# Kernel optimization log

Measured on AMD Instinct MI355X. Metric: run time of the kernel, lower is better.

Reference implementation:

```python
import jax, jax.numpy as jnp
import numpy as np

B, S, E, H = 4, 1024, 1024, 16
HD = E // H  # head_dim = 64
MAX_SEQ = 1024  # rel positions span [-(MAX_SEQ-1), MAX_SEQ-1]


def setup_inputs() -> dict:
    key = jax.random.key(0)
    ks = jax.random.split(key, 12)
    std_e = 1.0 / np.sqrt(E)
    std_h = 1.0 / np.sqrt(HD)
    inp = {
        "x": jax.random.normal(ks[0], (B, S, E), dtype=jnp.float32),
        # torch nn.Linear weights are [out, in]; y = x @ W.T + b
        "Wq": jax.random.uniform(ks[1], (E, E), jnp.float32, -std_e, std_e),
        "bq": jax.random.uniform(ks[2], (E,), jnp.float32, -std_e, std_e),
        "Wk": jax.random.uniform(ks[3], (E, E), jnp.float32, -std_e, std_e),
        "bk": jax.random.uniform(ks[4], (E,), jnp.float32, -std_e, std_e),
        "Wv": jax.random.uniform(ks[5], (E, E), jnp.float32, -std_e, std_e),
        "bv": jax.random.uniform(ks[6], (E,), jnp.float32, -std_e, std_e),
        "Wo": jax.random.uniform(ks[7], (E, E), jnp.float32, -std_e, std_e),
        "bo": jax.random.uniform(ks[8], (E,), jnp.float32, -std_e, std_e),
        # pos_key_proj: Linear(head_dim, head_dim, bias=False)
        "Wp": jax.random.uniform(ks[9], (HD, HD), jnp.float32, -std_h, std_h),
        # learned relative position table [2*max_seq_len-1, head_dim]
        "rel_table": jax.random.normal(ks[10], (2 * MAX_SEQ - 1, HD), dtype=jnp.float32),
    }
    return inp


def _rel_shift(pos_scores):
    # pos_scores: [B, H, S, 2S-1] -> [B, H, S, S]
    # result[..., i, j] = pos_scores[..., i, (S-1) - i + j]
    s = pos_scores.shape[-2]
    idx = (s - 1) - jnp.arange(s)[:, None] + jnp.arange(s)[None, :]  # [S, S]
    return jnp.take_along_axis(pos_scores, idx[None, None, :, :], axis=-1)


def reference(x, Wq, bq, Wk, bk, Wv, bv, Wo, bo, Wp, rel_table):
    scale = 1.0 / np.sqrt(HD)
    Q = (x @ Wq.T + bq).reshape(B, S, H, HD).transpose(0, 2, 1, 3)  # [B,H,S,HD]
    K = (x @ Wk.T + bk).reshape(B, S, H, HD).transpose(0, 2, 1, 3)
    V = (x @ Wv.T + bv).reshape(B, S, H, HD).transpose(0, 2, 1, 3)

    # rel_pos_encoding(S): slice centered at MAX_SEQ-1 covering 2S-1 positions
    center = MAX_SEQ - 1
    rel_emb = rel_table[center - (S - 1): center + S]  # [2S-1, HD]
    rel_key = rel_emb @ Wp.T                            # [2S-1, HD]

    content = jnp.einsum("bhqd,bhkd->bhqk", Q, K) * scale       # [B,H,S,S]
    pos = jnp.einsum("bhqd,pd->bhqp", Q, rel_key) * scale       # [B,H,S,2S-1]
    scores = content + _rel_shift(pos)                          # [B,H,S,S]

    probs = jax.nn.softmax(scores, axis=-1)
    ctx = jnp.einsum("bhqk,bhkd->bhqd", probs, V)               # [B,H,S,HD]
    ctx = ctx.transpose(0, 2, 1, 3).reshape(B, S, E)
    return ctx @ Wo.T + bo
```

## Files before the change

### kernel.cpp

```cpp
#include <hip/hip_runtime.h>
#include <hip/hip_bf16.h>

#define B_   4
#define S_   1024
#define E_   1024
#define H_   16
#define HD_  64

typedef float  f32x4  __attribute__((ext_vector_type(4)));
typedef short  bf16x8 __attribute__((ext_vector_type(8)));
typedef short  bf16x4 __attribute__((ext_vector_type(4)));

__device__ __forceinline__ float bf2f(short u) {
  union { unsigned int i; float f; } v;
  v.i = ((unsigned int)(unsigned short)u) << 16;
  return v.f;
}
__device__ __forceinline__ short f2bf(float f) {
  unsigned int x = __float_as_uint(f);
  x = x + 0x7fffu + ((x >> 16) & 1u);
  return (short)(x >> 16);
}
__device__ __forceinline__ bf16x8 ld_cvt8(const float* __restrict__ p) {
  const f32x4 a = *(const f32x4*)p;
  const f32x4 b = *(const f32x4*)(p + 4);
  bf16x8 r;
  r[0] = f2bf(a[0]); r[1] = f2bf(a[1]); r[2] = f2bf(a[2]); r[3] = f2bf(a[3]);
  r[4] = f2bf(b[0]); r[5] = f2bf(b[1]); r[6] = f2bf(b[2]); r[7] = f2bf(b[3]);
  return r;
}

__device__ __forceinline__ void gload_lds16(const short* g, short* l) {
  __builtin_amdgcn_global_load_lds(
      (const __attribute__((address_space(1))) void*)g,
      (__attribute__((address_space(3))) void*)l, 16, 0, 0);
}

__global__ __launch_bounds__(256) void cvt_f32_bf16(
    const float* __restrict__ src, short* __restrict__ dst, int n)
{
  const int i = (blockIdx.x * 256 + threadIdx.x) * 4;
  if (i < n) {
    const f32x4 v = *(const f32x4*)(src + i);
    bf16x4 o;
    o[0] = f2bf(v[0]); o[1] = f2bf(v[1]); o[2] = f2bf(v[2]); o[3] = f2bf(v[3]);
    *(bf16x4*)(dst + i) = o;
  }
}

__global__ __launch_bounds__(256) void cvt7_f32_bf16(
    const float* __restrict__ w0, const float* __restrict__ w1,
    const float* __restrict__ w2, const float* __restrict__ x,
    short* __restrict__ WB, short* __restrict__ xbf)
{
  const int NW = E_ * E_;
  const int y = blockIdx.y;
  const float* src;
  short* dst;
  if (y < 3) { src = (y == 0) ? w0 : (y == 1) ? w1 : w2; dst = WB + (size_t)y * NW; }
  else       { src = x + (size_t)(y - 3) * NW;           dst = xbf + (size_t)(y - 3) * NW; }
  const int i = (blockIdx.x * 256 + threadIdx.x) * 4;
  const f32x4 v = *(const f32x4*)(src + i);
  bf16x4 o;
  o[0] = f2bf(v[0]); o[1] = f2bf(v[1]); o[2] = f2bf(v[2]); o[3] = f2bf(v[3]);
  *(bf16x4*)(dst + i) = o;
}

template<int TM, int OUTF32>
__global__ __launch_bounds__(256) void gemm_bt(
    const short* __restrict__ A,
    const short* __restrict__ W0, const short* __restrict__ W1, const short* __restrict__ W2,
    const float* __restrict__ b0, const float* __restrict__ b1, const float* __restrict__ b2,
    void* __restrict__ C0v, void* __restrict__ C1v, void* __restrict__ C2v, int vz)
{
  constexpr int NJ = (TM == 128) ? 4 : 2;
  __shared__ short As[TM * 32];
  __shared__ short Bs[128 * 32];

  const int tid  = threadIdx.x;
  const int lane = tid & 63;
  const int wave = tid >> 6;
  const int quad = lane >> 4;
  const int l15  = lane & 15;
  const int wmb  = (TM == 128) ? (wave >> 1) * 64 : 0;
  const int wnb  = (TM == 128) ? (wave & 1) * 64 : wave * 32;
  const int m0   = blockIdx.y * TM;
  const int n0   = blockIdx.x * 128;
  const int z    = blockIdx.z;

  const short* W  = (z == 0) ? W0 : (z == 1) ? W1 : W2;
  const float* bb = (z == 0) ? b0 : (z == 1) ? b1 : b2;
  void*        Cv = (z == 0) ? C0v : (z == 1) ? C1v : C2v;

  const int trow = tid >> 2;
  const int tc   = tid & 3;

  f32x4 acc[4][NJ] = {};

  for (int k0 = 0; k0 < E_; k0 += 32) {
#pragma unroll
    for (int n = 0; n < TM / 64; ++n) {
      const int row  = trow + n * 64;
      const int srcc = tc ^ ((row >> 1) & 3);
      gload_lds16(A + (size_t)(m0 + row) * E_ + k0 + srcc * 8, &As[n * 2048 + tid * 8]);
    }
#pragma unroll
    for (int n = 0; n < 2; ++n) {
      const int row  = trow + n * 64;
      const int srcc = tc ^ ((row >> 1) & 3);
      gload_lds16(W + (size_t)(n0 + row) * E_ + k0 + srcc * 8, &Bs[n * 2048 + tid * 8]);
    }
    __syncthreads();

    bf16x8 af[4], bfr[NJ];
#pragma unroll
    for (int i = 0; i < 4; ++i) {
      const int row = wmb + i * 16 + l15;
      const int pc  = quad ^ ((row >> 1) & 3);
      af[i] = *(bf16x8*)&As[row * 32 + pc * 8];
    }
#pragma unroll
    for (int j = 0; j < NJ; ++j) {
      const int row = wnb + j * 16 + l15;
      const int pc  = quad ^ ((row >> 1) & 3);
      bfr[j] = *(bf16x8*)&Bs[row * 32 + pc * 8];
    }
#pragma unroll
    for (int i = 0; i < 4; ++i)
#pragma unroll
      for (int j = 0; j < NJ; ++j)
        acc[i][j] = __builtin_amdgcn_mfma_f32_16x16x32_bf16(af[i], bfr[j], acc[i][j], 0, 0, 0);
    __syncthreads();
  }

  if (TM == 128 && z == vz) {
    const int mtb = m0 + wmb;
    const int bq  = mtb >> 10;
    const int kt  = (mtb >> 6) & 15;
    short* Cs = (short*)Cv;
#pragma unroll
    for (int j = 0; j < NJ; ++j) {
      const int n = n0 + wnb + j * 16 + l15;
      const float bv = bb[n];
      const int h = (n >> 6) & 15;
      const int d = n & 63;
      bf16x8 lo, hi;
#pragma unroll
      for (int e = 0; e < 8; ++e) {
        lo[e] = f2bf(acc[e & 3][j][e >> 2] + bv);
        hi[e] = f2bf(acc[e & 3][j][(e >> 2) + 2] + bv);
      }
      const size_t off = ((size_t)((bq * 16 + h) * 64 + d)) * 1024 + kt * 64 + quad * 16;
      *(bf16x8*)(Cs + off)     = lo;
      *(bf16x8*)(Cs + off + 8) = hi;
    }
  } else {
#pragma unroll
    for (int j = 0; j < NJ; ++j) {
      const int n = n0 + wnb + j * 16 + l15;
      const float bv = bb[n];
#pragma unroll
      for (int i = 0; i < 4; ++i) {
        const int m = m0 + wmb + i * 16 + quad * 4;
#pragma unroll
        for (int r = 0; r < 4; ++r) {
          const float v = acc[i][j][r] + bv;
          if (OUTF32) ((float*)Cv)[(size_t)(m + r) * E_ + n] = v;
          else        ((short*)Cv)[(size_t)(m + r) * E_ + n] = f2bf(v);
        }
      }
    }
  }
}

__global__ __launch_bounds__(256) void relkey_mfma(
    const float* __restrict__ rel, const float* __restrict__ Wp, short* __restrict__ RKw)
{
  const int tid  = threadIdx.x;
  const int lane = tid & 63;
  const int wv   = tid >> 6;
  const int quad = lane >> 4;
  const int l15  = lane & 15;
  const int p0   = blockIdx.x * 64 + wv * 16;

  bf16x8 af[2];
  {
    int prow = p0 + l15; if (prow > 2046) prow = 2046;
    const float* ap = rel + (size_t)prow * 64 + quad * 8;
    af[0] = ld_cvt8(ap);
    af[1] = ld_cvt8(ap + 32);
  }
  f32x4 acc[4] = {};
#pragma unroll
  for (int nt = 0; nt < 4; ++nt) {
    const float* bp = Wp + (size_t)(nt * 16 + l15) * 64 + quad * 8;
    acc[nt] = __builtin_amdgcn_mfma_f32_16x16x32_bf16(af[0], ld_cvt8(bp),      acc[nt], 0, 0, 0);
    acc[nt] = __builtin_amdgcn_mfma_f32_16x16x32_bf16(af[1], ld_cvt8(bp + 32), acc[nt], 0, 0, 0);
  }
#pragma unroll
  for (int r = 0; r < 4; ++r) {
    const int p = p0 + quad * 4 + r;
    if (p < 2047)
#pragma unroll
      for (int nt = 0; nt < 4; ++nt)
        RKw[(size_t)p * 64 + nt * 16 + l15] = f2bf(acc[nt][r]);
  }
}

__global__ __launch_bounds__(512, 4) void attn_kernel(
    const short* __restrict__ Qw, const short* __restrict__ Kw,
    const short* __restrict__ Vtg, const short* __restrict__ RKw,
    short* __restrict__ Cw)
{
  __shared__ short Ks[64][72];
  __shared__ short Vt[64][72];
  __shared__ short RKs[256][72];
  __shared__ short Ps[8][16][72];

  const int tid  = threadIdx.x;
  const int lane = tid & 63;
  const int wv   = tid >> 6;
  const int quad = lane >> 4;
  const int l15  = lane & 15;

  const int lid  = blockIdx.x;
  const int pair = (lid & 7) * 8 + (lid >> 6);
  const int qt   = (lid >> 3) & 7;
  const int b    = pair >> 4;
  const int h    = pair & 15;
  const int bh   = pair;
  const int q0   = qt * 128;
  const int qw0  = q0 + wv * 16;
  const int jb   = 112 - 16 * wv;
  const int pbase0 = S_ - 128 - q0;

  bf16x8 qf[2];
  {
    const size_t base = (size_t)(b * S_ + qw0 + l15) * E_ + h * HD_ + quad * 8;
    qf[0] = *(const bf16x8*)(Qw + base);
    qf[1] = *(const bf16x8*)(Qw + base + 32);
  }

  f32x4 oacc[4] = {};
  float lsum[4] = {0.f, 0.f, 0.f, 0.f};

  const float fs = 0.125f * 1.44269504088896340736f;

  const int sr  = tid >> 3;
  const int sc8 = (tid & 7) * 8;

  {
    *(bf16x8*)&Ks[sr][sc8] =
        *(const bf16x8*)(Kw + (size_t)(b * S_ + sr) * E_ + h * HD_ + sc8);
    *(bf16x8*)&Vt[sr][sc8] =
        *(const bf16x8*)(Vtg + (size_t)(bh * 64 + sr) * 1024 + sc8);
#pragma unroll
    for (int jj = 0; jj < 3; ++jj) {
      const int c = tid + jj * 512;
      const int row = c >> 3, ch = (c & 7) * 8;
      int p = pbase0 + row; p = (p > 2046) ? 2046 : p;
      *(bf16x8*)&RKs[row][ch] = *(const bf16x8*)(RKw + (size_t)p * 64 + ch);
    }
    __syncthreads();
  }

#pragma unroll 1
  for (int kt = 0; kt < 16; ++kt) {
    bf16x8 kreg, vreg, rkreg;
    const bool havekv = (kt < 15);
    const bool haverk = (kt < 15);
    if (havekv) {
      kreg = *(const bf16x8*)(Kw + (size_t)(b * S_ + (kt + 1) * 64 + sr) * E_ + h * HD_ + sc8);
      vreg = *(const bf16x8*)(Vtg + (size_t)(bh * 64 + sr) * 1024 + (kt + 1) * 64 + sc8);
    }
    if (haverk) {
      int p = pbase0 + 64 * (kt + 3) + sr; if (p > 2046) p = 2046;
      rkreg = *(const bf16x8*)(RKw + (size_t)p * 64 + sc8);
    }

    f32x4 sc[4] = {};
#pragma unroll
    for (int s = 0; s < 2; ++s) {
#pragma unroll
      for (int kk = 0; kk < 4; ++kk) {
        bf16x8 bf = *(bf16x8*)&Ks[kk*16 + l15][s*32 + quad*8];
        sc[kk] = __builtin_amdgcn_mfma_f32_16x16x32_bf16(qf[s], bf, sc[kk], 0, 0, 0);
      }
    }

    f32x4 ta[5] = {};
#pragma unroll
    for (int jt = 0; jt < 5; ++jt) {
      const int off  = jb + jt * 16;
      const int slot = (kt + (off >> 6)) & 3;
      const int prow = slot * 64 + (off & 63);
#pragma unroll
      for (int s = 0; s < 2; ++s) {
        bf16x8 bf = *(bf16x8*)&RKs[prow + l15][s*32 + quad*8];
        ta[jt] = __builtin_amdgcn_mfma_f32_16x16x32_bf16(qf[s], bf, ta[jt], 0, 0, 0);
      }
    }

    float p[4][4];
#pragma unroll
    for (int r = 0; r < 4; ++r) {
      const int i16 = quad*4 + r;
      const int d   = 15 + l15 - i16;
      const int srcLane = (quad << 4) | (d & 15);
      float sj[5];
#pragma unroll
      for (int jt = 0; jt < 5; ++jt) sj[jt] = __shfl(ta[jt][r], srcLane, 64);
      const bool hi = (d >= 16);
#pragma unroll
      for (int kk = 0; kk < 4; ++kk) {
        const float t = hi ? sj[kk+1] : sj[kk];
        const float sv = fminf((sc[kk][r] + t) * fs, 108.f);
        const float pv = exp2f(sv - 12.f);
        p[kk][r] = pv;
        lsum[r] += pv;
      }
    }

#pragma unroll
    for (int r = 0; r < 4; ++r) {
      bf16x4 pw;
      pw[0] = f2bf(p[0][r]); pw[1] = f2bf(p[1][r]);
      pw[2] = f2bf(p[2][r]); pw[3] = f2bf(p[3][r]);
      *(bf16x4*)&Ps[wv][quad*4 + r][l15*4] = pw;
    }

#pragma unroll
    for (int ks = 0; ks < 2; ++ks) {
      bf16x8 pa = *(bf16x8*)&Ps[wv][l15][ks*32 + quad*8];
#pragma unroll
      for (int dt = 0; dt < 4; ++dt) {
        bf16x8 vb = *(bf16x8*)&Vt[dt*16 + l15][ks*32 + quad*8];
        oacc[dt] = __builtin_amdgcn_mfma_f32_16x16x32_bf16(pa, vb, oacc[dt], 0, 0, 0);
      }
    }

    __syncthreads();
    if (havekv) {
      *(bf16x8*)&Ks[sr][sc8] = kreg;
      *(bf16x8*)&Vt[sr][sc8] = vreg;
    }
    if (haverk) {
      *(bf16x8*)&RKs[((kt + 3) & 3) * 64 + sr][sc8] = rkreg;
    }
    __syncthreads();
  }

#pragma unroll
  for (int off = 1; off <= 8; off <<= 1)
#pragma unroll
    for (int r = 0; r < 4; ++r)
      lsum[r] += __shfl_xor(lsum[r], off, 64);

#pragma unroll
  for (int r = 0; r < 4; ++r) {
    const float inv = 1.0f / lsum[r];
    const size_t row = (size_t)(b * S_ + qw0 + quad*4 + r) * E_ + h * HD_;
#pragma unroll
    for (int dt = 0; dt < 4; ++dt)
      Cw[row + dt*16 + l15] = f2bf(oacc[dt][r] * inv);
  }
}

__global__ void fill_kernel(float* __restrict__ out, int n, float val) {
  for (int i = blockIdx.x * blockDim.x + threadIdx.x; i < n; i += gridDim.x * blockDim.x)
    out[i] = val;
}

extern "C" void kernel_launch(void* const* d_in, const int* in_sizes, int n_in,
                              void* d_out, int out_size, void* d_ws, size_t ws_size,
                              hipStream_t stream)
{
  const size_t WS_NEEDED = 33816448;
  if (ws_size < WS_NEEDED) {
    fill_kernel<<<1024, 256, 0, stream>>>((float*)d_out, out_size, 0.25f);
    return;
  }
  if (n_in != 11 || in_sizes[10] != 2047 * 64) {
    fill_kernel<<<1024, 256, 0, stream>>>((float*)d_out, out_size, 0.75f);
    return;
  }

  const float* x   = (const float*)d_in[0];
  const float* Wq  = (const float*)d_in[1];
  const float* bq  = (const float*)d_in[2];
  const float* Wk  = (const float*)d_in[3];
  const float* bk  = (const float*)d_in[4];
  const float* Wv  = (const float*)d_in[5];
  const float* bv  = (const float*)d_in[6];
  const float* Wo  = (const float*)d_in[7];
  const float* bo  = (const float*)d_in[8];
  const float* Wp  = (const float*)d_in[9];
  const float* rel = (const float*)d_in[10];

  char* ws = (char*)d_ws;
  short* Qws = (short*)(ws);
  short* Kws = (short*)(ws + 8388608);
  short* Vtg = (short*)(ws + 16777216);
  short* WB  = (short*)(ws + 25165824);
  short* ctx = (short*)(ws + 25165824);
  short* WoB = (short*)(ws + 8388608);
  short* RKw = (short*)(ws + 33554432);
  short* xbf = (short*)d_out;

  const int NW = E_ * E_;

  cvt7_f32_bf16<<<dim3(1024, 7), dim3(256), 0, stream>>>(Wq, Wk, Wv, x, WB, xbf);

  gemm_bt<128, 0><<<dim3(8, 32, 3), dim3(256), 0, stream>>>(
      xbf, WB, WB + NW, WB + 2 * NW, bq, bk, bv, Qws, Kws, Vtg, 2);

  relkey_mfma<<<dim3(32), dim3(256), 0, stream>>>(rel, Wp, RKw);

  attn_kernel<<<dim3(512), dim3(512), 0, stream>>>(Qws, Kws, Vtg, RKw, ctx);

  cvt_f32_bf16<<<dim3(NW / 1024), dim3(256), 0, stream>>>(Wo, WoB, NW);

  gemm_bt<64, 1><<<dim3(8, 64, 1), dim3(256), 0, stream>>>(
      ctx, WoB, WoB, WoB, bo, bo, bo, d_out, d_out, d_out, -1);
}
```

Baseline: 256.6 us.

## Fuse QKV projections into one GEMM sharing A tiles, swizzle block order

Replaces the three separate Q/K/V GEMM launches, indexed by blockIdx.z, with one kernel. Each block loads one 128-row tile of x and multiplies it against 64-column slices of all three weight matrices, so each A tile is reused three times instead of being reloaded per projection. Block indices are also remapped so neighbouring blocks share A rows for better L2 locality, and the output projection GEMM gets the same swizzled 1D grid. The cost is more accumulator registers per thread (3x4x2 tiles, launch bounds asking for 3 blocks per SM) and narrower N tiles per weight.

```diff
diff --git a/kernel.cpp b/kernel.cpp
--- a/kernel.cpp
+++ b/kernel.cpp
@@ -66,7 +66,113 @@
   *(bf16x4*)(dst + i) = o;
 }
 
-template<int TM, int OUTF32>
+__global__ __launch_bounds__(256, 3) void gemm_qkv(
+    const short* __restrict__ A, const short* __restrict__ W012,
+    const float* __restrict__ b0, const float* __restrict__ b1, const float* __restrict__ b2,
+    short* __restrict__ Qo, short* __restrict__ Ko, short* __restrict__ Vt)
+{
+  __shared__ short As[128 * 32];
+  __shared__ short Bs[3 * 64 * 32];
+
+  const int tid  = threadIdx.x;
+  const int lane = tid & 63;
+  const int wave = tid >> 6;
+  const int quad = lane >> 4;
+  const int l15  = lane & 15;
+  const int wmb  = (wave >> 1) * 64;
+  const int wnb  = (wave & 1) * 32;
+
+  const int lid = blockIdx.x;
+  const int m0  = ((lid & 7) * 4 + ((lid >> 3) & 3)) * 128;
+  const int n0  = (lid >> 5) * 64;
+
+  const int trow = tid >> 2;
+  const int tc   = tid & 3;
+
+  f32x4 acc[3][4][2] = {};
+
+  for (int k0 = 0; k0 < E_; k0 += 32) {
+#pragma unroll
+    for (int n = 0; n < 2; ++n) {
+      const int row  = trow + n * 64;
+      const int srcc = tc ^ ((row >> 1) & 3);
+      gload_lds16(A + (size_t)(m0 + row) * E_ + k0 + srcc * 8, &As[n * 2048 + tid * 8]);
+    }
+    {
+      const int srcc = tc ^ ((trow >> 1) & 3);
+#pragma unroll
+      for (int z = 0; z < 3; ++z)
+        gload_lds16(W012 + (size_t)z * E_ * E_ + (size_t)(n0 + trow) * E_ + k0 + srcc * 8,
+                    &Bs[z * 2048 + tid * 8]);
+    }
+    __syncthreads();
+
+    bf16x8 af[4];
+#pragma unroll
+    for (int i = 0; i < 4; ++i) {
+      const int row = wmb + i * 16 + l15;
+      const int pc  = quad ^ ((row >> 1) & 3);
+      af[i] = *(bf16x8*)&As[row * 32 + pc * 8];
+    }
+#pragma unroll
+    for (int z = 0; z < 3; ++z) {
+      bf16x8 bfr[2];
+#pragma unroll
+      for (int j = 0; j < 2; ++j) {
+        const int row = wnb + j * 16 + l15;
+        const int pc  = quad ^ ((row >> 1) & 3);
+        bfr[j] = *(bf16x8*)&Bs[z * 2048 + row * 32 + pc * 8];
+      }
+#pragma unroll
+      for (int i = 0; i < 4; ++i)
+#pragma unroll
+        for (int j = 0; j < 2; ++j)
+          acc[z][i][j] = __builtin_amdgcn_mfma_f32_16x16x32_bf16(af[i], bfr[j], acc[z][i][j], 0, 0, 0);
+    }
+    __syncthreads();
+  }
+
+#pragma unroll
+  for (int z = 0; z < 2; ++z) {
+    short* C = z ? Ko : Qo;
+    const float* bb = z ? b1 : b0;
+#pragma unroll
+    for (int j = 0; j < 2; ++j) {
+      const int n = n0 + wnb + j * 16 + l15;
+      const float bv = bb[n];
+#pragma unroll
+      for (int i = 0; i < 4; ++i) {
+        const int m = m0 + wmb + i * 16 + quad * 4;
+#pragma unroll
+        for (int r = 0; r < 4; ++r)
+          C[(size_t)(m + r) * E_ + n] = f2bf(acc[z][i][j][r] + bv);
+      }
+    }
+  }
+  {
+    const int mtb = m0 + wmb;
+    const int bq  = mtb >> 10;
+    const int kt  = (mtb >> 6) & 15;
+#pragma unroll
+    for (int j = 0; j < 2; ++j) {
+      const int n = n0 + wnb + j * 16 + l15;
+      const float bv = b2[n];
+      const int h = (n >> 6) & 15;
+      const int d = n & 63;
+      bf16x8 lo, hi;
+#pragma unroll
+      for (int e = 0; e < 8; ++e) {
+        lo[e] = f2bf(acc[2][e & 3][j][e >> 2] + bv);
+        hi[e] = f2bf(acc[2][e & 3][j][(e >> 2) + 2] + bv);
+      }
+      const size_t off = ((size_t)((bq * 16 + h) * 64 + d)) * 1024 + kt * 64 + quad * 16;
+      *(bf16x8*)(Vt + off)     = lo;
+      *(bf16x8*)(Vt + off + 8) = hi;
+    }
+  }
+}
+
+template<int TM, int OUTF32, int XSWZ>
 __global__ __launch_bounds__(256) void gemm_bt(
     const short* __restrict__ A,
     const short* __restrict__ W0, const short* __restrict__ W1, const short* __restrict__ W2,
@@ -84,9 +190,16 @@
   const int l15  = lane & 15;
   const int wmb  = (TM == 128) ? (wave >> 1) * 64 : 0;
   const int wnb  = (TM == 128) ? (wave & 1) * 64 : wave * 32;
-  const int m0   = blockIdx.y * TM;
-  const int n0   = blockIdx.x * 128;
-  const int z    = blockIdx.z;
+  int m0, n0;
+  if (XSWZ) {
+    const int lid = blockIdx.x;
+    m0 = ((lid & 7) * 8 + ((lid >> 3) & 7)) * TM;
+    n0 = (lid >> 6) * 128;
+  } else {
+    m0 = blockIdx.y * TM;
+    n0 = blockIdx.x * 128;
+  }
+  const int z = XSWZ ? 0 : blockIdx.z;
 
   const short* W  = (z == 0) ? W0 : (z == 1) ? W1 : W2;
   const float* bb = (z == 0) ? b0 : (z == 1) ? b1 : b2;
@@ -411,8 +524,8 @@
 
   cvt7_f32_bf16<<<dim3(1024, 7), dim3(256), 0, stream>>>(Wq, Wk, Wv, x, WB, xbf);
 
-  gemm_bt<128, 0><<<dim3(8, 32, 3), dim3(256), 0, stream>>>(
-      xbf, WB, WB + NW, WB + 2 * NW, bq, bk, bv, Qws, Kws, Vtg, 2);
+  gemm_qkv<<<dim3(512), dim3(256), 0, stream>>>(
+      xbf, WB, bq, bk, bv, Qws, Kws, Vtg);
 
   relkey_mfma<<<dim3(32), dim3(256), 0, stream>>>(rel, Wp, RKw);
 
@@ -420,6 +533,6 @@
 
   cvt_f32_bf16<<<dim3(NW / 1024), dim3(256), 0, stream>>>(Wo, WoB, NW);
 
-  gemm_bt<64, 1><<<dim3(8, 64, 1), dim3(256), 0, stream>>>(
+  gemm_bt<64, 1, 1><<<dim3(512), dim3(256), 0, stream>>>(
       ctx, WoB, WoB, WoB, bo, bo, bo, d_out, d_out, d_out, -1);
 }
```

Result: faster. 242.2 us (-5.6%).
